# Optimization experiments

Hardware: AMD Instinct MI355X
Metric: run time of the kernel (lower is better)

Reference implementation:

```python
import jax, jax.numpy as jnp
import numpy as np

B, S, IN = 32, 512, 19
DE, DD = 256, 128      # encoder / decoder d_model
HE, HD = 8, 4          # heads
LE, LD = 6, 2          # layers
FE, FD = 4 * DE, 4 * DD
EPS = 1e-5


def _ln(x, g, b):
    m = x.mean(-1, keepdims=True)
    v = ((x - m) ** 2).mean(-1, keepdims=True)
    return (x - m) / jnp.sqrt(v + EPS) * g + b


def _mha(x, qkv_w, qkv_b, out_w, out_b, kpad, nh):
    Bq, Sq, D = x.shape
    dh = D // nh
    qkv = x @ qkv_w.T + qkv_b
    q, k, v = jnp.split(qkv, 3, axis=-1)
    hs = lambda t: t.reshape(Bq, Sq, nh, dh).transpose(0, 2, 1, 3)  # -> [B,h,S,dh]
    q, k, v = hs(q), hs(k), hs(v)
    scores = jnp.einsum('bhqd,bhkd->bhqk', q, k) / float(np.sqrt(dh))
    scores = jnp.where(kpad[:, None, None, :], -1e9, scores)  # mask padded keys
    attn = jax.nn.softmax(scores, axis=-1)
    o = jnp.einsum('bhqk,bhkd->bhqd', attn, v).transpose(0, 2, 1, 3).reshape(Bq, Sq, D)
    return o @ out_w.T + out_b


def _block(x, p, kpad, nh):
    qkv_w, qkv_b, ow, ob, f1w, f1b, f2w, f2b, g1, b1, g2, b2 = p
    x = _ln(x + _mha(x, qkv_w, qkv_b, ow, ob, kpad, nh), g1, b1)
    h = jax.nn.relu(x @ f1w.T + f1b) @ f2w.T + f2b
    return _ln(x + h, g2, b2)


def _run(x, ps, kpad, nh, L):
    for i in range(L):
        x = _block(x, tuple(p[i] for p in ps), kpad, nh)
    return x


def _forward(event_tensor, w_in_enc, b_in_enc,
             enc_qkv_w, enc_qkv_b, enc_out_w, enc_out_b,
             enc_f1_w, enc_f1_b, enc_f2_w, enc_f2_b,
             enc_g1, enc_b1, enc_g2, enc_b2,
             mask_token, e2d_w,
             dec_qkv_w, dec_qkv_b, dec_out_w, dec_out_b,
             dec_f1_w, dec_f1_b, dec_f2_w, dec_f2_b,
             dec_g1, dec_b1, dec_g2, dec_b2,
             qh_w, qh_b, dth_w, dth_b,
             attention_mask, pred_mask):
    visible = attention_mask & (~pred_mask)
    counts = visible.sum(axis=1)                                  # [B]
    order = jnp.argsort(~visible, axis=1, stable=True)            # visible positions packed first, in order
    tok = event_tensor @ w_in_enc.T + b_in_enc                    # [B,S,DE]
    vis = jnp.take_along_axis(tok, order[:, :, None], axis=1)
    pos = jnp.arange(S)
    enc_pad = pos[None, :] >= counts[:, None]                      # True = padded slot
    vis = jnp.where(enc_pad[:, :, None], 0.0, vis)
    enc_ps = (enc_qkv_w, enc_qkv_b, enc_out_w, enc_out_b, enc_f1_w, enc_f1_b,
              enc_f2_w, enc_f2_b, enc_g1, enc_b1, enc_g2, enc_b2)
    enc_out = _run(vis, enc_ps, enc_pad, HE, LE)
    dec_vis = enc_out @ e2d_w.T                                    # [B,S,DD]
    idx = jnp.cumsum(visible.astype(jnp.int32), axis=1) - 1        # position -> packed index
    gathered = jnp.take_along_axis(dec_vis, jnp.clip(idx, 0)[:, :, None], axis=1)
    dec_in = jnp.where(visible[:, :, None], gathered, mask_token)  # mask token at masked/pad slots
    dec_ps = (dec_qkv_w, dec_qkv_b, dec_out_w, dec_out_b, dec_f1_w, dec_f1_b,
              dec_f2_w, dec_f2_b, dec_g1, dec_b1, dec_g2, dec_b2)
    dec_out = _run(dec_in, dec_ps, ~attention_mask, HD, LD)
    q = dec_out @ qh_w.T + qh_b
    dt = dec_out @ dth_w.T + dth_b
    return jnp.concatenate([q, dt], axis=-1)                       # [B,S,2]


def setup_inputs():
    key = jax.random.key(0)
    ks = iter(jax.random.split(key, 64))
    nrm = lambda shp, s=0.02: jax.random.normal(next(ks), shp, jnp.float32) * s
    d = {}
    d['event_tensor'] = jax.random.normal(next(ks), (B, S, IN), jnp.float32)
    lengths = jax.random.randint(next(ks), (B,), S // 2, S + 1)
    pos = jnp.arange(S)
    am = pos[None, :] < lengths[:, None]
    pm = (jax.random.uniform(next(ks), (B, S)) < 0.75) & am
    pm = pm.at[:, 0].set(False)  # guarantee >=1 visible token per row
    d['attention_mask'] = am
    d['pred_mask'] = pm
    d['w_in_enc'] = nrm((DE, IN)); d['b_in_enc'] = jnp.zeros((DE,), jnp.float32)
    d['enc_qkv_w'] = nrm((LE, 3 * DE, DE)); d['enc_qkv_b'] = jnp.zeros((LE, 3 * DE), jnp.float32)
    d['enc_out_w'] = nrm((LE, DE, DE));     d['enc_out_b'] = jnp.zeros((LE, DE), jnp.float32)
    d['enc_f1_w'] = nrm((LE, FE, DE));      d['enc_f1_b'] = jnp.zeros((LE, FE), jnp.float32)
    d['enc_f2_w'] = nrm((LE, DE, FE));      d['enc_f2_b'] = jnp.zeros((LE, DE), jnp.float32)
    d['enc_g1'] = jnp.ones((LE, DE), jnp.float32); d['enc_b1'] = jnp.zeros((LE, DE), jnp.float32)
    d['enc_g2'] = jnp.ones((LE, DE), jnp.float32); d['enc_b2'] = jnp.zeros((LE, DE), jnp.float32)
    d['mask_token'] = nrm((DD,))
    d['e2d_w'] = nrm((DD, DE))
    d['dec_qkv_w'] = nrm((LD, 3 * DD, DD)); d['dec_qkv_b'] = jnp.zeros((LD, 3 * DD), jnp.float32)
    d['dec_out_w'] = nrm((LD, DD, DD));     d['dec_out_b'] = jnp.zeros((LD, DD), jnp.float32)
    d['dec_f1_w'] = nrm((LD, FD, DD));      d['dec_f1_b'] = jnp.zeros((LD, FD), jnp.float32)
    d['dec_f2_w'] = nrm((LD, DD, FD));      d['dec_f2_b'] = jnp.zeros((LD, DD), jnp.float32)
    d['dec_g1'] = jnp.ones((LD, DD), jnp.float32); d['dec_b1'] = jnp.zeros((LD, DD), jnp.float32)
    d['dec_g2'] = jnp.ones((LD, DD), jnp.float32); d['dec_b2'] = jnp.zeros((LD, DD), jnp.float32)
    d['qh_w'] = nrm((1, DD));  d['qh_b'] = jnp.zeros((1,), jnp.float32)
    d['dth_w'] = nrm((1, DD)); d['dth_b'] = jnp.zeros((1,), jnp.float32)
    return d


def reference(event_tensor, attention_mask, pred_mask, w_in_enc, b_in_enc,
              enc_qkv_w, enc_qkv_b, enc_out_w, enc_out_b,
              enc_f1_w, enc_f1_b, enc_f2_w, enc_f2_b,
              enc_g1, enc_b1, enc_g2, enc_b2,
              mask_token, e2d_w,
              dec_qkv_w, dec_qkv_b, dec_out_w, dec_out_b,
              dec_f1_w, dec_f1_b, dec_f2_w, dec_f2_b,
              dec_g1, dec_b1, dec_g2, dec_b2,
              qh_w, qh_b, dth_w, dth_b):
    return _forward(event_tensor, w_in_enc, b_in_enc,
                    enc_qkv_w, enc_qkv_b, enc_out_w, enc_out_b,
                    enc_f1_w, enc_f1_b, enc_f2_w, enc_f2_b,
                    enc_g1, enc_b1, enc_g2, enc_b2,
                    mask_token, e2d_w,
                    dec_qkv_w, dec_qkv_b, dec_out_w, dec_out_b,
                    dec_f1_w, dec_f1_b, dec_f2_w, dec_f2_b,
                    dec_g1, dec_b1, dec_g2, dec_b2,
                    qh_w, qh_b, dth_w, dth_b,
                    attention_mask, pred_mask)
```

## Files before the change

kernel.cpp:

```cpp
#include <hip/hip_runtime.h>
#include <hip/hip_bf16.h>

#define B_ 32
#define S_ 512
#define IN_ 19
#define DE_ 256
#define DD_ 128
#define HE_ 8
#define HD_ 4
#define LE_ 6
#define LD_ 2
#define FE_ 1024
#define FD_ 512
#define DH_ 32

typedef __attribute__((ext_vector_type(8))) short short8;
typedef __attribute__((ext_vector_type(4))) float f32x4;

__device__ __forceinline__ short f2bf(float f) {
    union { float f; unsigned u; } x; x.f = f;
    unsigned r = x.u + 0x7fff + ((x.u >> 16) & 1);
    return (short)(r >> 16);
}
__device__ __forceinline__ float bf2f(short s) {
    union { unsigned u; float f; } x; x.u = ((unsigned)(unsigned short)s) << 16;
    return x.f;
}

#define GLL16(g, l) __builtin_amdgcn_global_load_lds( \
    (const __attribute__((address_space(1))) void*)(g), \
    (__attribute__((address_space(3))) void*)(l), 16, 0, 0)

#define QSCALE 0.2550653169f

#define NCONV 9
struct ConvTab {
    const float* src[NCONV];
    short* dst[NCONV];
    int len[NCONV];
};
__global__ __launch_bounds__(S_) void conv_plan_kernel(
    ConvTab tab, int total,
    const int* __restrict__ am, const int* __restrict__ pm,
    int* __restrict__ counts, int* __restrict__ lengths, int* __restrict__ order,
    int* __restrict__ visible, int* __restrict__ idx) {
    if (blockIdx.x < B_) {
        int b = blockIdx.x, s = threadIdx.x;
        __shared__ int sc[S_];
        int a = (am[b * S_ + s] != 0);
        int v = a && (pm[b * S_ + s] == 0);
        visible[b * S_ + s] = v;
        sc[s] = v | (a << 16);
        __syncthreads();
#pragma unroll
        for (int off = 1; off < S_; off <<= 1) {
            int t = (s >= off) ? sc[s - off] : 0;
            __syncthreads();
            sc[s] += t;
            __syncthreads();
        }
        int incl = sc[s] & 0xffff;
        int tot = sc[S_ - 1];
        int total2 = tot & 0xffff;
        if (s == 0) { counts[b] = total2; lengths[b] = tot >> 16; }
        idx[b * S_ + s] = (incl > 0) ? incl - 1 : 0;
        if (v) order[b * S_ + incl - 1] = s;
        else   order[b * S_ + total2 + (s - incl)] = s;
    } else {
        int i = (blockIdx.x - B_) * S_ + threadIdx.x;
        if (i >= total) return;
        int j = i;
        for (int e = 0; e < NCONV; ++e) {
            if (j < tab.len[e]) { tab.dst[e][j] = f2bf(tab.src[e][j]); return; }
            j -= tab.len[e];
        }
    }
}

__global__ __launch_bounds__(DE_) void enc_embed_kernel(
    const float* __restrict__ ev, const float* __restrict__ w, const float* __restrict__ bias,
    const int* __restrict__ counts, const int* __restrict__ order, short* __restrict__ out) {
    int bs = blockIdx.x;
    int b = bs / S_, s = bs % S_;
    int d = threadIdx.x;
    __shared__ float e[IN_];
    bool padded = (s >= counts[b]);
    int src = order[bs];
    if (threadIdx.x < IN_)
        e[threadIdx.x] = padded ? 0.f : ev[(size_t)(b * S_ + src) * IN_ + threadIdx.x];
    __syncthreads();
    float acc = bias[d];
#pragma unroll
    for (int i = 0; i < IN_; ++i) acc += e[i] * w[d * IN_ + i];
    out[(size_t)bs * DE_ + d] = padded ? f2bf(0.f) : f2bf(acc);
}

template <int TM, int TN, bool RELU, bool QKV>
__global__ __launch_bounds__(256) void gemm_mfma(
    const short* __restrict__ A, const short* __restrict__ Wt, const float* __restrict__ bias,
    short* __restrict__ C, int M, int N, int K,
    short* __restrict__ qb, short* __restrict__ kb, short* __restrict__ vtb, int H, int D,
    const int* __restrict__ live) {
    constexpr int HM = TM / 2, HN = TN / 2;
    constexpr int MI = HM / 16, NI = HN / 16;
    constexpr int NCHA = TM / 16, NCH = (TM + TN) / 16;
    int bm = blockIdx.y * TM, bn = blockIdx.x * TN;
    if (live && (bm & (S_ - 1)) >= live[bm >> 9]) return;
    __shared__ short As[TM][32];
    __shared__ short Bs[TN][32];
    int t = threadIdx.x;
    int wave = t >> 6, lane = t & 63;
    int wm = (wave >> 1) * HM, wn = (wave & 1) * HN;
    int c = lane & 15, quad = lane >> 4;
    f32x4 acc[MI][NI];
#pragma unroll
    for (int i = 0; i < MI; ++i)
#pragma unroll
        for (int j = 0; j < NI; ++j) acc[i][j] = (f32x4){0.f, 0.f, 0.f, 0.f};

    int srow = lane >> 2, scol = (lane & 3) * 8;

    for (int k0 = 0; k0 < K; k0 += 32) {
#pragma unroll
        for (int ch0 = 0; ch0 < NCH; ch0 += 4) {
            int ch = ch0 + wave;
            if (ch < NCHA)
                GLL16(A + (size_t)(bm + ch * 16 + srow) * K + k0 + scol, &As[ch * 16][0]);
            else
                GLL16(Wt + (size_t)(bn + (ch - NCHA) * 16 + srow) * K + k0 + scol,
                      &Bs[(ch - NCHA) * 16][0]);
        }
        __syncthreads();
        short8 av[MI], bv[NI];
#pragma unroll
        for (int mi = 0; mi < MI; ++mi) av[mi] = *(const short8*)&As[wm + mi * 16 + c][quad * 8];
#pragma unroll
        for (int ni = 0; ni < NI; ++ni) bv[ni] = *(const short8*)&Bs[wn + ni * 16 + c][quad * 8];
#pragma unroll
        for (int mi = 0; mi < MI; ++mi)
#pragma unroll
            for (int ni = 0; ni < NI; ++ni)
                acc[mi][ni] = __builtin_amdgcn_mfma_f32_16x16x32_bf16(av[mi], bv[ni], acc[mi][ni], 0, 0, 0);
        __syncthreads();
    }
#pragma unroll
    for (int mi = 0; mi < MI; ++mi)
#pragma unroll
        for (int ni = 0; ni < NI; ++ni)
#pragma unroll
            for (int r = 0; r < 4; ++r) {
                int R = bm + wm + mi * 16 + quad * 4 + r;
                int Ncol = bn + wn + ni * 16 + c;
                float v = acc[mi][ni][r] + (bias ? bias[Ncol] : 0.f);
                if (RELU) v = fmaxf(v, 0.f);
                if (!QKV) {
                    C[(size_t)R * N + Ncol] = f2bf(v);
                } else {
                    int s = R & (S_ - 1), b2 = R >> 9;
                    if (Ncol < D) {
                        int h = Ncol >> 5, d = Ncol & 31;
                        qb[(((size_t)b2 * H + h) * S_ + s) * DH_ + d] = f2bf(v * QSCALE);
                    } else if (Ncol < 2 * D) {
                        int n2 = Ncol - D, h = n2 >> 5, d = n2 & 31;
                        kb[(((size_t)b2 * H + h) * S_ + s) * DH_ + d] = f2bf(v);
                    } else {
                        int n2 = Ncol - 2 * D, h = n2 >> 5, d = n2 & 31;
                        vtb[(((size_t)b2 * H + h) * DH_ + d) * S_ + s] = f2bf(v);
                    }
                }
            }
}

__global__ __launch_bounds__(256) void attn_flash(
    const short* __restrict__ qb, const short* __restrict__ kb, const short* __restrict__ vtb,
    const int* __restrict__ limit_arr, const int* __restrict__ qlim,
    short* __restrict__ o, int H, int D) {
    int b = blockIdx.z, h = blockIdx.y;
    if (qlim && (int)(blockIdx.x * 64) >= qlim[b]) return;
    int wave = threadIdx.x >> 6, lane = threadIdx.x & 63;
    int q0 = blockIdx.x * 64 + wave * 16;
    int c = lane & 15, quad = lane >> 4;
    size_t bh = (size_t)b * H + h;
    __shared__ short PtAll[4][16][132];
    short (*Pt)[132] = PtAll[wave];

    f32x4 zero = (f32x4){0.f, 0.f, 0.f, 0.f};
    short8 aq = *(const short8*)&qb[(bh * S_ + q0 + c) * DH_ + quad * 8];
    const short* kbase = kb + bh * S_ * DH_;
    const short* vbase = vtb + bh * DH_ * S_;

    int limit = limit_arr[b];
    int nchunks = (limit + 127) >> 7;

    float lrow[4] = {0.f, 0.f, 0.f, 0.f};
    f32x4 o0 = zero, o1 = zero;

    for (int kc = 0; kc < nchunks; ++kc) {
        f32x4 s[8];
#pragma unroll
        for (int nt = 0; nt < 8; ++nt) {
            short8 bk = *(const short8*)&kbase[(size_t)(kc * 128 + nt * 16 + c) * DH_ + quad * 8];
            s[nt] = __builtin_amdgcn_mfma_f32_16x16x32_bf16(aq, bk, zero, 0, 0, 0);
        }
#pragma unroll
        for (int nt = 0; nt < 8; ++nt) {
            bool ok = (kc * 128 + nt * 16 + c) < limit;
#pragma unroll
            for (int r = 0; r < 4; ++r) {
                float p = ok ? exp2f(s[nt][r]) : 0.f;
                s[nt][r] = p;
                lrow[r] += p;
            }
        }
#pragma unroll
        for (int nt = 0; nt < 8; ++nt)
#pragma unroll
            for (int r = 0; r < 4; ++r)
                Pt[quad * 4 + r][nt * 16 + c] = f2bf(s[nt][r]);
#pragma unroll
        for (int kk = 0; kk < 4; ++kk) {
            short8 ap = *(const short8*)&Pt[c][kk * 32 + quad * 8];
            short8 b0 = *(const short8*)&vbase[(size_t)c * S_ + kc * 128 + kk * 32 + quad * 8];
            short8 b1 = *(const short8*)&vbase[(size_t)(16 + c) * S_ + kc * 128 + kk * 32 + quad * 8];
            o0 = __builtin_amdgcn_mfma_f32_16x16x32_bf16(ap, b0, o0, 0, 0, 0);
            o1 = __builtin_amdgcn_mfma_f32_16x16x32_bf16(ap, b1, o1, 0, 0, 0);
        }
    }
#pragma unroll
    for (int r = 0; r < 4; ++r) {
        float l = lrow[r];
        l += __shfl_xor(l, 1);
        l += __shfl_xor(l, 2);
        l += __shfl_xor(l, 4);
        l += __shfl_xor(l, 8);
        float inv = 1.f / l;
        int row = quad * 4 + r;
        size_t base = (size_t)(b * S_ + q0 + row) * D + h * DH_;
        o[base + c] = f2bf(o0[r] * inv);
        o[base + 16 + c] = f2bf(o1[r] * inv);
    }
}

template <int D>
__global__ __launch_bounds__(64) void add_ln_kernel(
    const short* __restrict__ x, const short* __restrict__ h,
    const float* __restrict__ g, const float* __restrict__ be,
    short* __restrict__ out, const int* __restrict__ live) {
    constexpr int E = D / 64;
    int row = blockIdx.x, t = threadIdx.x;
    if (live && (row & (S_ - 1)) >= live[row >> 9]) return;
    const short* px = x + (size_t)row * D + t * E;
    const short* ph = h + (size_t)row * D + t * E;
    float v[E];
    float s = 0.f;
#pragma unroll
    for (int e = 0; e < E; ++e) {
        v[e] = bf2f(px[e]) + bf2f(ph[e]);
        s += v[e];
    }
#pragma unroll
    for (int off = 32; off; off >>= 1) s += __shfl_xor(s, off, 64);
    float m = s / D;
    float s2 = 0.f;
#pragma unroll
    for (int e = 0; e < E; ++e) {
        float d = v[e] - m;
        s2 += d * d;
    }
#pragma unroll
    for (int off = 32; off; off >>= 1) s2 += __shfl_xor(s2, off, 64);
    float rstd = rsqrtf(s2 / D + 1e-5f);
    short* po = out + (size_t)row * D + t * E;
#pragma unroll
    for (int e = 0; e < E; ++e)
        po[e] = f2bf((v[e] - m) * rstd * g[t * E + e] + be[t * E + e]);
}

__global__ __launch_bounds__(64) void add_ln_head_kernel(
    const short* __restrict__ x, const short* __restrict__ h,
    const float* __restrict__ g, const float* __restrict__ be,
    const float* __restrict__ qw, const float* __restrict__ qb,
    const float* __restrict__ dw, const float* __restrict__ db,
    float* __restrict__ out) {
    int row = blockIdx.x, t = threadIdx.x;
    int d0 = t * 2, d1 = t * 2 + 1;
    float v0 = bf2f(x[(size_t)row * DD_ + d0]) + bf2f(h[(size_t)row * DD_ + d0]);
    float v1 = bf2f(x[(size_t)row * DD_ + d1]) + bf2f(h[(size_t)row * DD_ + d1]);
    float s = v0 + v1;
#pragma unroll
    for (int off = 32; off; off >>= 1) s += __shfl_xor(s, off, 64);
    float m = s / DD_;
    float a0 = v0 - m, a1 = v1 - m;
    float s2 = a0 * a0 + a1 * a1;
#pragma unroll
    for (int off = 32; off; off >>= 1) s2 += __shfl_xor(s2, off, 64);
    float rstd = rsqrtf(s2 / DD_ + 1e-5f);
    float o0 = a0 * rstd * g[d0] + be[d0];
    float o1 = a1 * rstd * g[d1] + be[d1];
    float q = o0 * qw[d0] + o1 * qw[d1];
    float dt = o0 * dw[d0] + o1 * dw[d1];
#pragma unroll
    for (int off = 32; off; off >>= 1) {
        q += __shfl_xor(q, off, 64);
        dt += __shfl_xor(dt, off, 64);
    }
    if (t == 0) {
        out[(size_t)row * 2 + 0] = q + qb[0];
        out[(size_t)row * 2 + 1] = dt + db[0];
    }
}

__global__ __launch_bounds__(DD_) void dec_embed_kernel(
    const short* __restrict__ dec_vis, const float* __restrict__ mask_token,
    const int* __restrict__ visible, const int* __restrict__ idx, short* __restrict__ out) {
    int bs = blockIdx.x, d = threadIdx.x;
    int b = bs / S_;
    short val = visible[bs] ? dec_vis[(size_t)(b * S_ + idx[bs]) * DD_ + d]
                            : f2bf(mask_token[d]);
    out[(size_t)bs * DD_ + d] = val;
}

extern "C" void kernel_launch(void* const* d_in, const int* in_sizes, int n_in,
                              void* d_out, int out_size, void* d_ws, size_t ws_size,
                              hipStream_t stream) {
    const float* ev      = (const float*)d_in[0];
    const int*  am       = (const int*)d_in[1];
    const int*  pm       = (const int*)d_in[2];
    const float* w_in    = (const float*)d_in[3];
    const float* b_in    = (const float*)d_in[4];
    const float* eqkv_w  = (const float*)d_in[5];
    const float* eqkv_b  = (const float*)d_in[6];
    const float* eout_w  = (const float*)d_in[7];
    const float* eout_b  = (const float*)d_in[8];
    const float* ef1_w   = (const float*)d_in[9];
    const float* ef1_b   = (const float*)d_in[10];
    const float* ef2_w   = (const float*)d_in[11];
    const float* ef2_b   = (const float*)d_in[12];
    const float* eg1     = (const float*)d_in[13];
    const float* eb1     = (const float*)d_in[14];
    const float* eg2     = (const float*)d_in[15];
    const float* eb2     = (const float*)d_in[16];
    const float* mask_tok= (const float*)d_in[17];
    const float* e2d_w   = (const float*)d_in[18];
    const float* dqkv_w  = (const float*)d_in[19];
    const float* dqkv_b  = (const float*)d_in[20];
    const float* dout_w  = (const float*)d_in[21];
    const float* dout_b  = (const float*)d_in[22];
    const float* df1_w   = (const float*)d_in[23];
    const float* df1_b   = (const float*)d_in[24];
    const float* df2_w   = (const float*)d_in[25];
    const float* df2_b   = (const float*)d_in[26];
    const float* dg1     = (const float*)d_in[27];
    const float* db1     = (const float*)d_in[28];
    const float* dg2     = (const float*)d_in[29];
    const float* db2     = (const float*)d_in[30];
    const float* qh_w    = (const float*)d_in[31];
    const float* qh_b    = (const float*)d_in[32];
    const float* dth_w   = (const float*)d_in[33];
    const float* dth_b   = (const float*)d_in[34];
    float* out = (float*)d_out;

    const int BS = B_ * S_;
    char* ws = (char*)d_ws;
    int* counts  = (int*)ws;
    int* lengths = counts + 32;
    int* order   = lengths + 32;
    int* visible = order + BS;
    int* idx     = visible + BS;

    short* wb = (short*)(ws + 256 * 1024);
    const int L_eqkv = LE_ * 3 * DE_ * DE_;
    const int L_eout = LE_ * DE_ * DE_;
    const int L_ef1  = LE_ * FE_ * DE_;
    const int L_ef2  = LE_ * DE_ * FE_;
    const int L_e2d  = DD_ * DE_;
    const int L_dqkv = LD_ * 3 * DD_ * DD_;
    const int L_dout = LD_ * DD_ * DD_;
    const int L_df1  = LD_ * FD_ * DD_;
    const int L_df2  = LD_ * DD_ * FD_;
    short* w_eqkv = wb;
    short* w_eout = w_eqkv + L_eqkv;
    short* w_ef1  = w_eout + L_eout;
    short* w_ef2  = w_ef1 + L_ef1;
    short* w_e2d  = w_ef2 + L_ef2;
    short* w_dqkv = w_e2d + L_e2d;
    short* w_dout = w_dqkv + L_dqkv;
    short* w_df1  = w_dout + L_dout;
    short* w_df2  = w_df1 + L_df1;
    const int convTotal = L_eqkv + L_eout + L_ef1 + L_ef2 + L_e2d + L_dqkv + L_dout + L_df1 + L_df2;

    short* bx    = (short*)(ws + 12 * 1024 * 1024);
    short* qbuf  = bx   + (size_t)BS * DE_;
    short* kbuf  = qbuf + (size_t)B_ * HE_ * S_ * DH_;
    short* vtbuf = kbuf + (size_t)B_ * HE_ * S_ * DH_;
    short* battn = vtbuf + (size_t)B_ * HE_ * S_ * DH_;
    short* bt    = battn + (size_t)BS * DE_;
    short* hid   = bt + (size_t)BS * DE_;

    ConvTab tab;
    tab.src[0] = eqkv_w; tab.dst[0] = w_eqkv; tab.len[0] = L_eqkv;
    tab.src[1] = eout_w; tab.dst[1] = w_eout; tab.len[1] = L_eout;
    tab.src[2] = ef1_w;  tab.dst[2] = w_ef1;  tab.len[2] = L_ef1;
    tab.src[3] = ef2_w;  tab.dst[3] = w_ef2;  tab.len[3] = L_ef2;
    tab.src[4] = e2d_w;  tab.dst[4] = w_e2d;  tab.len[4] = L_e2d;
    tab.src[5] = dqkv_w; tab.dst[5] = w_dqkv; tab.len[5] = L_dqkv;
    tab.src[6] = dout_w; tab.dst[6] = w_dout; tab.len[6] = L_dout;
    tab.src[7] = df1_w;  tab.dst[7] = w_df1;  tab.len[7] = L_df1;
    tab.src[8] = df2_w;  tab.dst[8] = w_df2;  tab.len[8] = L_df2;
    conv_plan_kernel<<<B_ + (convTotal + S_ - 1) / S_, S_, 0, stream>>>(
        tab, convTotal, am, pm, counts, lengths, order, visible, idx);
    enc_embed_kernel<<<BS, DE_, 0, stream>>>(ev, w_in, b_in, counts, order, bx);

    for (int l = 0; l < LE_; ++l) {
        gemm_mfma<64, 64, false, true><<<dim3(3 * DE_ / 64, BS / 64), 256, 0, stream>>>(
            bx, w_eqkv + (size_t)l * 3 * DE_ * DE_, eqkv_b + (size_t)l * 3 * DE_,
            nullptr, BS, 3 * DE_, DE_, qbuf, kbuf, vtbuf, HE_, DE_, counts);
        attn_flash<<<dim3(S_ / 64, HE_, B_), 256, 0, stream>>>(
            qbuf, kbuf, vtbuf, counts, counts, battn, HE_, DE_);
        gemm_mfma<32, 32, false, false><<<dim3(DE_ / 32, BS / 32), 256, 0, stream>>>(
            battn, w_eout + (size_t)l * DE_ * DE_, eout_b + (size_t)l * DE_,
            bt, BS, DE_, DE_, nullptr, nullptr, nullptr, 0, 0, counts);
        add_ln_kernel<DE_><<<BS, 64, 0, stream>>>(
            bx, bt, eg1 + (size_t)l * DE_, eb1 + (size_t)l * DE_, bx, counts);
        gemm_mfma<64, 64, true, false><<<dim3(FE_ / 64, BS / 64), 256, 0, stream>>>(
            bx, w_ef1 + (size_t)l * FE_ * DE_, ef1_b + (size_t)l * FE_,
            hid, BS, FE_, DE_, nullptr, nullptr, nullptr, 0, 0, counts);
        gemm_mfma<32, 32, false, false><<<dim3(DE_ / 32, BS / 32), 256, 0, stream>>>(
            hid, w_ef2 + (size_t)l * DE_ * FE_, ef2_b + (size_t)l * DE_,
            bt, BS, DE_, FE_, nullptr, nullptr, nullptr, 0, 0, counts);
        add_ln_kernel<DE_><<<BS, 64, 0, stream>>>(
            bx, bt, eg2 + (size_t)l * DE_, eb2 + (size_t)l * DE_, bx, counts);
    }

    gemm_mfma<32, 32, false, false><<<dim3(DD_ / 32, BS / 32), 256, 0, stream>>>(
        bx, w_e2d, nullptr, bt, BS, DD_, DE_, nullptr, nullptr, nullptr, 0, 0, counts);
    dec_embed_kernel<<<BS, DD_, 0, stream>>>(bt, mask_tok, visible, idx, bx);

    for (int l = 0; l < LD_; ++l) {
        gemm_mfma<64, 64, false, true><<<dim3(3 * DD_ / 64, BS / 64), 256, 0, stream>>>(
            bx, w_dqkv + (size_t)l * 3 * DD_ * DD_, dqkv_b + (size_t)l * 3 * DD_, nullptr,
            BS, 3 * DD_, DD_, qbuf, kbuf, vtbuf, HD_, DD_, nullptr);
        attn_flash<<<dim3(S_ / 64, HD_, B_), 256, 0, stream>>>(
            qbuf, kbuf, vtbuf, lengths, nullptr, battn, HD_, DD_);
        gemm_mfma<32, 32, false, false><<<dim3(DD_ / 32, BS / 32), 256, 0, stream>>>(
            battn, w_dout + (size_t)l * DD_ * DD_, dout_b + (size_t)l * DD_,
            bt, BS, DD_, DD_, nullptr, nullptr, nullptr, 0, 0, nullptr);
        add_ln_kernel<DD_><<<BS, 64, 0, stream>>>(
            bx, bt, dg1 + (size_t)l * DD_, db1 + (size_t)l * DD_, bx, nullptr);
        gemm_mfma<64, 64, true, false><<<dim3(FD_ / 64, BS / 64), 256, 0, stream>>>(
            bx, w_df1 + (size_t)l * FD_ * DD_, df1_b + (size_t)l * FD_,
            hid, BS, FD_, DD_, nullptr, nullptr, nullptr, 0, 0, nullptr);
        gemm_mfma<32, 32, false, false><<<dim3(DD_ / 32, BS / 32), 256, 0, stream>>>(
            hid, w_df2 + (size_t)l * DD_ * FD_, df2_b + (size_t)l * DD_,
            bt, BS, DD_, FD_, nullptr, nullptr, nullptr, 0, 0, nullptr);
        if (l < LD_ - 1) {
            add_ln_kernel<DD_><<<BS, 64, 0, stream>>>(
                bx, bt, dg2 + (size_t)l * DD_, db2 + (size_t)l * DD_, bx, nullptr);
        } else {
            add_ln_head_kernel<<<BS, 64, 0, stream>>>(
                bx, bt, dg2 + (size_t)l * DD_, db2 + (size_t)l * DD_,
                qh_w, qh_b, dth_w, dth_b, out);
        }
    }
}
```

Before: 872.3 us.

## Fuse output/FFN2 GEMMs with residual LayerNorm and double-buffer GEMM tiles

```diff
diff --git a/kernel.cpp b/kernel.cpp
--- a/kernel.cpp
+++ b/kernel.cpp
@@ -106,8 +106,8 @@
     constexpr int NCHA = TM / 16, NCH = (TM + TN) / 16;
     int bm = blockIdx.y * TM, bn = blockIdx.x * TN;
     if (live && (bm & (S_ - 1)) >= live[bm >> 9]) return;
-    __shared__ short As[TM][32];
-    __shared__ short Bs[TN][32];
+    __shared__ short As[2][TM][32];
+    __shared__ short Bs[2][TN][32];
     int t = threadIdx.x;
     int wave = t >> 6, lane = t & 63;
     int wm = (wave >> 1) * HM, wn = (wave & 1) * HN;
@@ -119,23 +119,30 @@
         for (int j = 0; j < NI; ++j) acc[i][j] = (f32x4){0.f, 0.f, 0.f, 0.f};
 
     int srow = lane >> 2, scol = (lane & 3) * 8;
-
-    for (int k0 = 0; k0 < K; k0 += 32) {
+    int nk = K >> 5;
+
+    auto stage = [&](int buf, int k0) {
 #pragma unroll
         for (int ch0 = 0; ch0 < NCH; ch0 += 4) {
             int ch = ch0 + wave;
             if (ch < NCHA)
-                GLL16(A + (size_t)(bm + ch * 16 + srow) * K + k0 + scol, &As[ch * 16][0]);
-            else
+                GLL16(A + (size_t)(bm + ch * 16 + srow) * K + k0 + scol, &As[buf][ch * 16][0]);
+            else if (ch < NCH)
                 GLL16(Wt + (size_t)(bn + (ch - NCHA) * 16 + srow) * K + k0 + scol,
-                      &Bs[(ch - NCHA) * 16][0]);
-        }
-        __syncthreads();
+                      &Bs[buf][(ch - NCHA) * 16][0]);
+        }
+    };
+
+    stage(0, 0);
+    __syncthreads();
+    for (int kt = 0; kt < nk; ++kt) {
+        int cur = kt & 1;
+        if (kt + 1 < nk) stage(cur ^ 1, (kt + 1) << 5);
         short8 av[MI], bv[NI];
 #pragma unroll
-        for (int mi = 0; mi < MI; ++mi) av[mi] = *(const short8*)&As[wm + mi * 16 + c][quad * 8];
-#pragma unroll
-        for (int ni = 0; ni < NI; ++ni) bv[ni] = *(const short8*)&Bs[wn + ni * 16 + c][quad * 8];
+        for (int mi = 0; mi < MI; ++mi) av[mi] = *(const short8*)&As[cur][wm + mi * 16 + c][quad * 8];
+#pragma unroll
+        for (int ni = 0; ni < NI; ++ni) bv[ni] = *(const short8*)&Bs[cur][wn + ni * 16 + c][quad * 8];
 #pragma unroll
         for (int mi = 0; mi < MI; ++mi)
 #pragma unroll
@@ -171,6 +178,126 @@
             }
 }
 
+template <int N, bool HEAD>
+__global__ __launch_bounds__(256) void gemm_ln(
+    const short* __restrict__ A, const short* __restrict__ Wt,
+    const float* __restrict__ bias, const short* x ,
+    const float* __restrict__ g, const float* __restrict__ be,
+    short* out,
+    const float* __restrict__ qw, const float* __restrict__ qbb,
+    const float* __restrict__ dw, const float* __restrict__ dbb,
+    float* __restrict__ outf,
+    int K, const int* __restrict__ live) {
+    constexpr int TM = 32;
+    constexpr int HN = N / 2, NI = HN / 16;
+    constexpr int NCHA = TM / 16, NCH = NCHA + N / 16;
+    constexpr int HST = N + 8;
+    constexpr int BUF = (TM + N) * 32;
+    int bm = blockIdx.x * TM;
+    if (live && (bm & (S_ - 1)) >= live[bm >> 9]) return;
+    __shared__ short smem[2 * BUF];
+    int t = threadIdx.x, wave = t >> 6, lane = t & 63;
+    int wm = (wave >> 1) * 16, wn = (wave & 1) * HN;
+    int c = lane & 15, quad = lane >> 4;
+    int srow = lane >> 2, scol = (lane & 3) * 8;
+    f32x4 acc[NI];
+#pragma unroll
+    for (int ni = 0; ni < NI; ++ni) acc[ni] = (f32x4){0.f, 0.f, 0.f, 0.f};
+    int nk = K >> 5;
+
+    auto stage = [&](int buf, int k0) {
+        short* base = smem + buf * BUF;
+#pragma unroll
+        for (int ch0 = 0; ch0 < NCH; ch0 += 4) {
+            int ch = ch0 + wave;
+            if (ch < NCHA)
+                GLL16(A + (size_t)(bm + ch * 16 + srow) * K + k0 + scol, base + ch * 16 * 32);
+            else if (ch < NCH)
+                GLL16(Wt + (size_t)((ch - NCHA) * 16 + srow) * K + k0 + scol,
+                      base + (TM + (ch - NCHA) * 16) * 32);
+        }
+    };
+
+    stage(0, 0);
+    __syncthreads();
+    for (int kt = 0; kt < nk; ++kt) {
+        int cur = kt & 1;
+        if (kt + 1 < nk) stage(cur ^ 1, (kt + 1) << 5);
+        const short* base = smem + cur * BUF;
+        short8 av = *(const short8*)(base + (wm + c) * 32 + quad * 8);
+        short8 bv[NI];
+#pragma unroll
+        for (int ni = 0; ni < NI; ++ni)
+            bv[ni] = *(const short8*)(base + (TM + wn + ni * 16 + c) * 32 + quad * 8);
+#pragma unroll
+        for (int ni = 0; ni < NI; ++ni)
+            acc[ni] = __builtin_amdgcn_mfma_f32_16x16x32_bf16(av, bv[ni], acc[ni], 0, 0, 0);
+        __syncthreads();
+    }
+
+    short* Hs = smem;
+#pragma unroll
+    for (int ni = 0; ni < NI; ++ni) {
+        int col = wn + ni * 16 + c;
+        float bcol = bias[col];
+#pragma unroll
+        for (int r = 0; r < 4; ++r)
+            Hs[(wm + quad * 4 + r) * HST + col] = f2bf(acc[ni][r] + bcol);
+    }
+    __syncthreads();
+
+    constexpr int CPL = N / 8;
+    int r = t >> 3, li = t & 7;
+    int R = bm + r;
+    int c0 = li * CPL;
+    float v[CPL];
+    float s = 0.f;
+#pragma unroll
+    for (int e8 = 0; e8 < CPL / 8; ++e8) {
+        short8 xv = *(const short8*)&x[(size_t)R * N + c0 + e8 * 8];
+#pragma unroll
+        for (int j = 0; j < 8; ++j) {
+            float vv = bf2f(xv[j]) + bf2f(Hs[r * HST + c0 + e8 * 8 + j]);
+            v[e8 * 8 + j] = vv;
+            s += vv;
+        }
+    }
+    s += __shfl_xor(s, 1); s += __shfl_xor(s, 2); s += __shfl_xor(s, 4);
+    float m = s / N;
+    float s2 = 0.f;
+#pragma unroll
+    for (int e = 0; e < CPL; ++e) { float d = v[e] - m; s2 += d * d; }
+    s2 += __shfl_xor(s2, 1); s2 += __shfl_xor(s2, 2); s2 += __shfl_xor(s2, 4);
+    float rstd = rsqrtf(s2 / N + 1e-5f);
+    if (!HEAD) {
+        if (live && ((R & (S_ - 1)) >= live[R >> 9])) return;
+#pragma unroll
+        for (int e8 = 0; e8 < CPL / 8; ++e8) {
+            short8 ov;
+#pragma unroll
+            for (int j = 0; j < 8; ++j) {
+                int e = e8 * 8 + j;
+                ov[j] = f2bf((v[e] - m) * rstd * g[c0 + e] + be[c0 + e]);
+            }
+            *(short8*)&out[(size_t)R * N + c0 + e8 * 8] = ov;
+        }
+    } else {
+        float q = 0.f, dt = 0.f;
+#pragma unroll
+        for (int e = 0; e < CPL; ++e) {
+            float o = (v[e] - m) * rstd * g[c0 + e] + be[c0 + e];
+            q += o * qw[c0 + e];
+            dt += o * dw[c0 + e];
+        }
+        q += __shfl_xor(q, 1); q += __shfl_xor(q, 2); q += __shfl_xor(q, 4);
+        dt += __shfl_xor(dt, 1); dt += __shfl_xor(dt, 2); dt += __shfl_xor(dt, 4);
+        if (li == 0) {
+            outf[(size_t)R * 2 + 0] = q + qbb[0];
+            outf[(size_t)R * 2 + 1] = dt + dbb[0];
+        }
+    }
+}
+
 __global__ __launch_bounds__(256) void attn_flash(
     const short* __restrict__ qb, const short* __restrict__ kb, const short* __restrict__ vtb,
     const int* __restrict__ limit_arr, const int* __restrict__ qlim,
@@ -238,75 +365,6 @@
         size_t base = (size_t)(b * S_ + q0 + row) * D + h * DH_;
         o[base + c] = f2bf(o0[r] * inv);
         o[base + 16 + c] = f2bf(o1[r] * inv);
-    }
-}
-
-template <int D>
-__global__ __launch_bounds__(64) void add_ln_kernel(
-    const short* __restrict__ x, const short* __restrict__ h,
-    const float* __restrict__ g, const float* __restrict__ be,
-    short* __restrict__ out, const int* __restrict__ live) {
-    constexpr int E = D / 64;
-    int row = blockIdx.x, t = threadIdx.x;
-    if (live && (row & (S_ - 1)) >= live[row >> 9]) return;
-    const short* px = x + (size_t)row * D + t * E;
-    const short* ph = h + (size_t)row * D + t * E;
-    float v[E];
-    float s = 0.f;
-#pragma unroll
-    for (int e = 0; e < E; ++e) {
-        v[e] = bf2f(px[e]) + bf2f(ph[e]);
-        s += v[e];
-    }
-#pragma unroll
-    for (int off = 32; off; off >>= 1) s += __shfl_xor(s, off, 64);
-    float m = s / D;
-    float s2 = 0.f;
-#pragma unroll
-    for (int e = 0; e < E; ++e) {
-        float d = v[e] - m;
-        s2 += d * d;
-    }
-#pragma unroll
-    for (int off = 32; off; off >>= 1) s2 += __shfl_xor(s2, off, 64);
-    float rstd = rsqrtf(s2 / D + 1e-5f);
-    short* po = out + (size_t)row * D + t * E;
-#pragma unroll
-    for (int e = 0; e < E; ++e)
-        po[e] = f2bf((v[e] - m) * rstd * g[t * E + e] + be[t * E + e]);
-}
-
-__global__ __launch_bounds__(64) void add_ln_head_kernel(
-    const short* __restrict__ x, const short* __restrict__ h,
-    const float* __restrict__ g, const float* __restrict__ be,
-    const float* __restrict__ qw, const float* __restrict__ qb,
-    const float* __restrict__ dw, const float* __restrict__ db,
-    float* __restrict__ out) {
-    int row = blockIdx.x, t = threadIdx.x;
-    int d0 = t * 2, d1 = t * 2 + 1;
-    float v0 = bf2f(x[(size_t)row * DD_ + d0]) + bf2f(h[(size_t)row * DD_ + d0]);
-    float v1 = bf2f(x[(size_t)row * DD_ + d1]) + bf2f(h[(size_t)row * DD_ + d1]);
-    float s = v0 + v1;
-#pragma unroll
-    for (int off = 32; off; off >>= 1) s += __shfl_xor(s, off, 64);
-    float m = s / DD_;
-    float a0 = v0 - m, a1 = v1 - m;
-    float s2 = a0 * a0 + a1 * a1;
-#pragma unroll
-    for (int off = 32; off; off >>= 1) s2 += __shfl_xor(s2, off, 64);
-    float rstd = rsqrtf(s2 / DD_ + 1e-5f);
-    float o0 = a0 * rstd * g[d0] + be[d0];
-    float o1 = a1 * rstd * g[d1] + be[d1];
-    float q = o0 * qw[d0] + o1 * qw[d1];
-    float dt = o0 * dw[d0] + o1 * dw[d1];
-#pragma unroll
-    for (int off = 32; off; off >>= 1) {
-        q += __shfl_xor(q, off, 64);
-        dt += __shfl_xor(dt, off, 64);
-    }
-    if (t == 0) {
-        out[(size_t)row * 2 + 0] = q + qb[0];
-        out[(size_t)row * 2 + 1] = dt + db[0];
     }
 }
 
@@ -417,19 +475,17 @@
             nullptr, BS, 3 * DE_, DE_, qbuf, kbuf, vtbuf, HE_, DE_, counts);
         attn_flash<<<dim3(S_ / 64, HE_, B_), 256, 0, stream>>>(
             qbuf, kbuf, vtbuf, counts, counts, battn, HE_, DE_);
-        gemm_mfma<32, 32, false, false><<<dim3(DE_ / 32, BS / 32), 256, 0, stream>>>(
+        gemm_ln<DE_, false><<<BS / 32, 256, 0, stream>>>(
             battn, w_eout + (size_t)l * DE_ * DE_, eout_b + (size_t)l * DE_,
-            bt, BS, DE_, DE_, nullptr, nullptr, nullptr, 0, 0, counts);
-        add_ln_kernel<DE_><<<BS, 64, 0, stream>>>(
-            bx, bt, eg1 + (size_t)l * DE_, eb1 + (size_t)l * DE_, bx, counts);
+            bx, eg1 + (size_t)l * DE_, eb1 + (size_t)l * DE_, bx,
+            nullptr, nullptr, nullptr, nullptr, nullptr, DE_, counts);
         gemm_mfma<64, 64, true, false><<<dim3(FE_ / 64, BS / 64), 256, 0, stream>>>(
             bx, w_ef1 + (size_t)l * FE_ * DE_, ef1_b + (size_t)l * FE_,
             hid, BS, FE_, DE_, nullptr, nullptr, nullptr, 0, 0, counts);
-        gemm_mfma<32, 32, false, false><<<dim3(DE_ / 32, BS / 32), 256, 0, stream>>>(
+        gemm_ln<DE_, false><<<BS / 32, 256, 0, stream>>>(
             hid, w_ef2 + (size_t)l * DE_ * FE_, ef2_b + (size_t)l * DE_,
-            bt, BS, DE_, FE_, nullptr, nullptr, nullptr, 0, 0, counts);
-        add_ln_kernel<DE_><<<BS, 64, 0, stream>>>(
-            bx, bt, eg2 + (size_t)l * DE_, eb2 + (size_t)l * DE_, bx, counts);
+            bx, eg2 + (size_t)l * DE_, eb2 + (size_t)l * DE_, bx,
+            nullptr, nullptr, nullptr, nullptr, nullptr, FE_, counts);
     }
 
     gemm_mfma<32, 32, false, false><<<dim3(DD_ / 32, BS / 32), 256, 0, stream>>>(
@@ -442,24 +498,23 @@
             BS, 3 * DD_, DD_, qbuf, kbuf, vtbuf, HD_, DD_, nullptr);
         attn_flash<<<dim3(S_ / 64, HD_, B_), 256, 0, stream>>>(
             qbuf, kbuf, vtbuf, lengths, nullptr, battn, HD_, DD_);
-        gemm_mfma<32, 32, false, false><<<dim3(DD_ / 32, BS / 32), 256, 0, stream>>>(
+        gemm_ln<DD_, false><<<BS / 32, 256, 0, stream>>>(
             battn, w_dout + (size_t)l * DD_ * DD_, dout_b + (size_t)l * DD_,
-            bt, BS, DD_, DD_, nullptr, nullptr, nullptr, 0, 0, nullptr);
-        add_ln_kernel<DD_><<<BS, 64, 0, stream>>>(
-            bx, bt, dg1 + (size_t)l * DD_, db1 + (size_t)l * DD_, bx, nullptr);
+            bx, dg1 + (size_t)l * DD_, db1 + (size_t)l * DD_, bx,
+            nullptr, nullptr, nullptr, nullptr, nullptr, DD_, nullptr);
         gemm_mfma<64, 64, true, false><<<dim3(FD_ / 64, BS / 64), 256, 0, stream>>>(
             bx, w_df1 + (size_t)l * FD_ * DD_, df1_b + (size_t)l * FD_,
             hid, BS, FD_, DD_, nullptr, nullptr, nullptr, 0, 0, nullptr);
-        gemm_mfma<32, 32, false, false><<<dim3(DD_ / 32, BS / 32), 256, 0, stream>>>(
-            hid, w_df2 + (size_t)l * DD_ * FD_, df2_b + (size_t)l * DD_,
-            bt, BS, DD_, FD_, nullptr, nullptr, nullptr, 0, 0, nullptr);
         if (l < LD_ - 1) {
-            add_ln_kernel<DD_><<<BS, 64, 0, stream>>>(
-                bx, bt, dg2 + (size_t)l * DD_, db2 + (size_t)l * DD_, bx, nullptr);
+            gemm_ln<DD_, false><<<BS / 32, 256, 0, stream>>>(
+                hid, w_df2 + (size_t)l * DD_ * FD_, df2_b + (size_t)l * DD_,
+                bx, dg2 + (size_t)l * DD_, db2 + (size_t)l * DD_, bx,
+                nullptr, nullptr, nullptr, nullptr, nullptr, FD_, nullptr);
         } else {
-            add_ln_head_kernel<<<BS, 64, 0, stream>>>(
-                bx, bt, dg2 + (size_t)l * DD_, db2 + (size_t)l * DD_,
-                qh_w, qh_b, dth_w, dth_b, out);
-        }
-    }
-}
+            gemm_ln<DD_, true><<<BS / 32, 256, 0, stream>>>(
+                hid, w_df2 + (size_t)l * DD_ * FD_, df2_b + (size_t)l * DD_,
+                bx, dg2 + (size_t)l * DD_, db2 + (size_t)l * DD_, nullptr,
+                qh_w, qh_b, dth_w, dth_b, out, FD_, nullptr);
+        }
+    }
+}
```

New measurement: 855.6 us. No clear change (-1.9%).
